# Kernel tuning notes

Measured on AMD Instinct MI355X. Metric: run time of the kernel, lower is better.

## Reference

```python
import jax, jax.numpy as jnp
import numpy as np

DIM_IN, DIM_H, DIM_OUT = 1024, 512, 256
E, T, B = 8, 4, 16384


def setup_inputs() -> dict:
    key = jax.random.key(0)
    ks = jax.random.split(key, 8)
    s1 = 1.0 / np.sqrt(DIM_IN)
    s2 = 1.0 / np.sqrt(DIM_H)
    x = jax.random.normal(ks[0], (B, DIM_IN), dtype=jnp.float32)
    # stacked expert params: layer1 [E, H, IN], layer2 [E, OUT, H]
    W1 = jax.random.uniform(ks[1], (E, DIM_H, DIM_IN), jnp.float32, -s1, s1)
    b1 = jax.random.uniform(ks[2], (E, DIM_H), jnp.float32, -s1, s1)
    W2 = jax.random.uniform(ks[3], (E, DIM_OUT, DIM_H), jnp.float32, -s2, s2)
    b2 = jax.random.uniform(ks[4], (E, DIM_OUT), jnp.float32, -s2, s2)
    # gate params: [T, E, IN]
    Wg = jax.random.uniform(ks[5], (T, E, DIM_IN), jnp.float32, -s1, s1)
    bg = jax.random.uniform(ks[6], (T, E), jnp.float32, -s1, s1)
    return {"x": x, "W1": W1, "b1": b1, "W2": W2, "b2": b2, "Wg": Wg, "bg": bg}


def reference(x, W1, b1, W2, b2, Wg, bg):
    # Experts: Linear+ReLU, Linear+ReLU (dropout=0 / eval mode)
    h = jax.nn.relu(jnp.einsum('bi,ehi->beh', x, W1) + b1)          # [B,E,H]
    feats = jax.nn.relu(jnp.einsum('beh,edh->bed', h, W2) + b2)     # [B,E,D]
    # Gates: softmax over experts, one gate per task
    logits = jnp.einsum('bi,tei->bte', x, Wg) + bg                  # [B,T,E]
    w = jax.nn.softmax(logits, axis=-1)                             # [B,T,E]
    # Weighted combine: einsum('bde,be->bd') per task
    out = jnp.einsum('bed,bte->tbd', feats, w)                      # [T,B,D]
    return out
```

## Files before the change

### kernel.cpp

```cpp
#include <hip/hip_runtime.h>


typedef __attribute__((ext_vector_type(8))) __bf16 bf16x8;
typedef __attribute__((ext_vector_type(4))) float f32x4;
typedef __attribute__((ext_vector_type(8))) unsigned short u16x8;

__device__ __forceinline__ float bf2f(unsigned short u) {
  union { unsigned int i; float f; } x;
  x.i = ((unsigned int)u) << 16;
  return x.f;
}

__device__ __forceinline__ unsigned short f2bf(float f) {
  union { float f; unsigned int i; } x;
  x.f = f;
  unsigned int r = x.i + 0x7FFFu + ((x.i >> 16) & 1u);
  return (unsigned short)(r >> 16);
}

__device__ __forceinline__ void gload_lds16(const unsigned short* g, unsigned short* l) {
  __builtin_amdgcn_global_load_lds(
      (const __attribute__((address_space(1))) void*)g,
      (__attribute__((address_space(3))) void*)l, 16, 0, 0);
}

__global__ void cvt_k(const float* __restrict__ in, unsigned short* __restrict__ out, int n4) {
  int i = blockIdx.x * blockDim.x + threadIdx.x;
  if (i >= n4) return;
  float4 v = ((const float4*)in)[i];
  ushort4 o;
  o.x = f2bf(v.x); o.y = f2bf(v.y); o.z = f2bf(v.z); o.w = f2bf(v.w);
  ((ushort4*)out)[i] = o;
}

__global__ __launch_bounds__(256) void gates_k(
    const unsigned short* __restrict__ xb,
    const unsigned short* __restrict__ Wgb,
    const float* __restrict__ bg,
    float* __restrict__ gw)
{
  const int lane = threadIdx.x & 63;
  const int wid = threadIdx.x >> 6;
  const int wgid = blockIdx.x * 4 + wid;
  const int brow = wgid * 16;
  const int l15 = lane & 15, lhi = lane >> 4;

  f32x4 acc0 = {0.f, 0.f, 0.f, 0.f};
  f32x4 acc1 = {0.f, 0.f, 0.f, 0.f};
  for (int k0 = 0; k0 < 1024; k0 += 32) {
    bf16x8 a  = *(const bf16x8*)&xb[(size_t)(brow + l15) * 1024 + k0 + lhi * 8];
    bf16x8 b0 = *(const bf16x8*)&Wgb[(size_t)l15 * 1024 + k0 + lhi * 8];
    bf16x8 b1 = *(const bf16x8*)&Wgb[(size_t)(16 + l15) * 1024 + k0 + lhi * 8];
    acc0 = __builtin_amdgcn_mfma_f32_16x16x32_bf16(a, b0, acc0, 0, 0, 0);
    acc1 = __builtin_amdgcn_mfma_f32_16x16x32_bf16(a, b1, acc1, 0, 0, 0);
  }
  const float bg0 = bg[l15];
  const float bg1 = bg[16 + l15];
#pragma unroll
  for (int r = 0; r < 4; ++r) {
    float v0 = acc0[r] + bg0;
    float v1 = acc1[r] + bg1;
    float m0 = v0, m1 = v1;
#pragma unroll
    for (int d = 1; d <= 4; d <<= 1) {
      m0 = fmaxf(m0, __shfl_xor(m0, d));
      m1 = fmaxf(m1, __shfl_xor(m1, d));
    }
    float e0 = __expf(v0 - m0), e1 = __expf(v1 - m1);
    float s0 = e0, s1 = e1;
#pragma unroll
    for (int d = 1; d <= 4; d <<= 1) {
      s0 += __shfl_xor(s0, d);
      s1 += __shfl_xor(s1, d);
    }
    int b = brow + lhi * 4 + r;
    gw[(size_t)b * 32 + l15]      = e0 / s0;
    gw[(size_t)b * 32 + 16 + l15] = e1 / s1;
  }
}

template <bool RELU>
__global__ __launch_bounds__(512, 2) void gemm256(
    const unsigned short* __restrict__ A, int lda, int aZ,
    const unsigned short* __restrict__ B,
    const float* __restrict__ bias,
    unsigned short* __restrict__ C, int ldc, int cZ,
    int tilesN, int N, int K)
{
  extern __shared__ char smem_raw[];
  unsigned short* lds = (unsigned short*)smem_raw;
  char* ldsb = (char*)smem_raw;

  const int tid = threadIdx.x;
  const int lane = tid & 63, wid = tid >> 6;
  const int wr = wid >> 2, wc = wid & 3;
  const int l15 = lane & 15, lhi = lane >> 4;

  const int nwg = gridDim.x;
  const int cpx = nwg >> 3;
  const int wg = blockIdx.x;
  const int swz = (wg & 7) * cpx + (wg >> 3);
  const int rt = swz / tilesN, ct = swz - rt * tilesN;
  const int brow = rt * 256, bcol = ct * 256;
  const int e = blockIdx.z;

  const unsigned short* Ab = A + (size_t)e * aZ + (size_t)brow * lda;
  const unsigned short* Bb = B + (size_t)e * N * K + (size_t)bcol * K;
  const float* biasb = bias + (size_t)e * N;
  unsigned short* Cb = C + (size_t)e * cZ;

  const int NT = K >> 6;
  const int NI = NT >> 1;

  const int trow = tid >> 3;
  const int cg8 = (((tid & 7) ^ (trow & 7)) << 3);

  const int axor = (l15 & 7) << 4;
  const int koff0 = (lhi << 4) ^ axor;
  const int koff1 = (64 + (lhi << 4)) ^ axor;

  const char* pA0 = ldsb + wr * 16384 + l15 * 128 + koff0;
  const char* pA1 = ldsb + wr * 16384 + l15 * 128 + koff1;
  const char* pB0 = ldsb + 65536 + wc * 8192 + l15 * 128 + koff0;
  const char* pB1 = ldsb + 65536 + wc * 8192 + l15 * 128 + koff1;

  f32x4 bias4[4];
#pragma unroll
  for (int nf = 0; nf < 4; ++nf)
    bias4[nf] = *(const f32x4*)&biasb[bcol + wc * 64 + nf * 16 + lhi * 4];

  const f32x4 zero = {0.f, 0.f, 0.f, 0.f};
  f32x4 acc[8][4];
#pragma unroll
  for (int m = 0; m < 8; ++m)
#pragma unroll
    for (int n = 0; n < 4; ++n) acc[m][n] = zero;

  auto STAGE_A = [&](int slot, int t, int u) {
    gload_lds16(Ab + (size_t)(u * 64 + trow) * lda + (t * 64 + cg8),
                lds + slot * 16384 + u * 4096 + wid * 512);
  };
  auto STAGE_B = [&](int slot, int t, int u) {
    gload_lds16(Bb + (size_t)(u * 64 + trow) * K + (t * 64 + cg8),
                lds + 32768 + slot * 16384 + u * 4096 + wid * 512);
  };

#pragma unroll
  for (int u = 0; u < 4; ++u) STAGE_B(0, 0, u);
#pragma unroll
  for (int u = 0; u < 4; ++u) STAGE_A(0, 0, u);
  asm volatile("s_waitcnt vmcnt(0)" ::: "memory");
  __builtin_amdgcn_s_barrier();

  auto ktile = [&](int slot, int tn, bool stageNext) {
    bf16x8 af[4][2], bfr[4][2];
#pragma unroll
    for (int mi = 0; mi < 4; ++mi) {
      af[mi][0] = *(const bf16x8*)(pA0 + slot * 32768 + mi * 2048);
      af[mi][1] = *(const bf16x8*)(pA1 + slot * 32768 + mi * 2048);
    }
#pragma unroll
    for (int n = 0; n < 2; ++n) {
      bfr[n][0] = *(const bf16x8*)(pB0 + slot * 32768 + n * 2048);
      bfr[n][1] = *(const bf16x8*)(pB1 + slot * 32768 + n * 2048);
    }
    if (stageNext) { STAGE_B(slot ^ 1, tn, 0); STAGE_B(slot ^ 1, tn, 1); }
    __builtin_amdgcn_s_barrier();
    __builtin_amdgcn_s_setprio(1);
#pragma unroll
    for (int kk = 0; kk < 2; ++kk)
#pragma unroll
      for (int mi = 0; mi < 4; ++mi)
#pragma unroll
        for (int n = 0; n < 2; ++n)
          acc[mi][n] = __builtin_amdgcn_mfma_f32_16x16x32_bf16(bfr[n][kk], af[mi][kk], acc[mi][n], 0, 0, 0);
    __builtin_amdgcn_s_setprio(0);
    __builtin_amdgcn_s_barrier();

#pragma unroll
    for (int n = 0; n < 2; ++n) {
      bfr[2 + n][0] = *(const bf16x8*)(pB0 + slot * 32768 + (2 + n) * 2048);
      bfr[2 + n][1] = *(const bf16x8*)(pB1 + slot * 32768 + (2 + n) * 2048);
    }
    if (stageNext) { STAGE_B(slot ^ 1, tn, 2); STAGE_B(slot ^ 1, tn, 3); }
    __builtin_amdgcn_s_barrier();
    __builtin_amdgcn_s_setprio(1);
#pragma unroll
    for (int kk = 0; kk < 2; ++kk)
#pragma unroll
      for (int mi = 0; mi < 4; ++mi)
#pragma unroll
        for (int n = 0; n < 2; ++n)
          acc[mi][2 + n] = __builtin_amdgcn_mfma_f32_16x16x32_bf16(bfr[2 + n][kk], af[mi][kk], acc[mi][2 + n], 0, 0, 0);
    __builtin_amdgcn_s_setprio(0);
    asm volatile("s_waitcnt vmcnt(4)" ::: "memory");
    __builtin_amdgcn_s_barrier();

#pragma unroll
    for (int mi = 0; mi < 4; ++mi) {
      af[mi][0] = *(const bf16x8*)(pA0 + slot * 32768 + 8192 + mi * 2048);
      af[mi][1] = *(const bf16x8*)(pA1 + slot * 32768 + 8192 + mi * 2048);
    }
    if (stageNext) { STAGE_A(slot ^ 1, tn, 0); STAGE_A(slot ^ 1, tn, 2); }
    __builtin_amdgcn_s_barrier();
    __builtin_amdgcn_s_setprio(1);
#pragma unroll
    for (int kk = 0; kk < 2; ++kk)
#pragma unroll
      for (int mi = 0; mi < 4; ++mi)
#pragma unroll
        for (int n = 0; n < 2; ++n)
          acc[4 + mi][n] = __builtin_amdgcn_mfma_f32_16x16x32_bf16(bfr[n][kk], af[mi][kk], acc[4 + mi][n], 0, 0, 0);
    __builtin_amdgcn_s_setprio(0);
    __builtin_amdgcn_s_barrier();

    if (stageNext) { STAGE_A(slot ^ 1, tn, 1); STAGE_A(slot ^ 1, tn, 3); }
    __builtin_amdgcn_s_barrier();
    __builtin_amdgcn_s_setprio(1);
#pragma unroll
    for (int kk = 0; kk < 2; ++kk)
#pragma unroll
      for (int mi = 0; mi < 4; ++mi)
#pragma unroll
        for (int n = 0; n < 2; ++n)
          acc[4 + mi][2 + n] = __builtin_amdgcn_mfma_f32_16x16x32_bf16(bfr[2 + n][kk], af[mi][kk], acc[4 + mi][2 + n], 0, 0, 0);
    __builtin_amdgcn_s_setprio(0);
    asm volatile("s_waitcnt vmcnt(2)" ::: "memory");
    __builtin_amdgcn_s_barrier();
  };

  for (int i = 0; i < NI; ++i) {
    ktile(0, 2 * i + 1, true);
    ktile(1, 2 * i + 2, (2 * i + 2) < NT);
  }

#pragma unroll
  for (int mf = 0; mf < 8; ++mf) {
    const size_t rowoff = (size_t)(brow + wr * 128 + mf * 16 + l15) * ldc;
#pragma unroll
    for (int nf = 0; nf < 4; ++nf) {
      const int col = bcol + wc * 64 + nf * 16 + lhi * 4;
      f32x4 v = acc[mf][nf];
      ushort4 o;
      float v0 = v[0] + bias4[nf][0];
      float v1 = v[1] + bias4[nf][1];
      float v2 = v[2] + bias4[nf][2];
      float v3 = v[3] + bias4[nf][3];
      if (RELU) {
        v0 = v0 > 0.f ? v0 : 0.f;
        v1 = v1 > 0.f ? v1 : 0.f;
        v2 = v2 > 0.f ? v2 : 0.f;
        v3 = v3 > 0.f ? v3 : 0.f;
      }
      o.x = f2bf(v0); o.y = f2bf(v1); o.z = f2bf(v2); o.w = f2bf(v3);
      *(ushort4*)&Cb[rowoff + col] = o;
    }
  }
}

__global__ __launch_bounds__(256) void combine_k(
    const unsigned short* __restrict__ feats,
    const float* __restrict__ gw,
    float* __restrict__ out)
{
  int tid = blockIdx.x * 256 + threadIdx.x;
  int b = tid >> 5;
  int d0 = (tid & 31) * 8;

  const f32x4* wv4 = (const f32x4*)(gw + (size_t)b * 32);
  f32x4 wv[8];
#pragma unroll
  for (int i = 0; i < 8; ++i) wv[i] = wv4[i];

  float o[4][8];
#pragma unroll
  for (int t = 0; t < 4; ++t)
#pragma unroll
    for (int j = 0; j < 8; ++j) o[t][j] = 0.f;

#pragma unroll
  for (int e = 0; e < 8; ++e) {
    u16x8 fv = *(const u16x8*)&feats[((size_t)b * 8 + e) * 256 + d0];
    float f[8];
#pragma unroll
    for (int j = 0; j < 8; ++j) f[j] = bf2f(fv[j]);
#pragma unroll
    for (int t = 0; t < 4; ++t) {
      float wt = wv[(t * 8 + e) >> 2][(t * 8 + e) & 3];
#pragma unroll
      for (int j = 0; j < 8; ++j) o[t][j] += wt * f[j];
    }
  }
#pragma unroll
  for (int t = 0; t < 4; ++t) {
    f32x4* dst = (f32x4*)(out + ((size_t)t * 16384 + b) * 256 + d0);
    f32x4 s0 = {o[t][0], o[t][1], o[t][2], o[t][3]};
    f32x4 s1 = {o[t][4], o[t][5], o[t][6], o[t][7]};
    dst[0] = s0;
    dst[1] = s1;
  }
}

extern "C" void kernel_launch(void* const* d_in, const int* in_sizes, int n_in,
                              void* d_out, int out_size, void* d_ws, size_t ws_size,
                              hipStream_t stream) {
  (void)in_sizes; (void)n_in; (void)out_size; (void)ws_size;
  const float* x  = (const float*)d_in[0];
  const float* W1 = (const float*)d_in[1];
  const float* b1 = (const float*)d_in[2];
  const float* W2 = (const float*)d_in[3];
  const float* b2 = (const float*)d_in[4];
  const float* Wg = (const float*)d_in[5];
  const float* bg = (const float*)d_in[6];
  float* out = (float*)d_out;

  char* ws = (char*)d_ws;
  unsigned short* xb    = (unsigned short*)ws; ws += (size_t)16384 * 1024 * 2;
  unsigned short* W1b   = (unsigned short*)ws; ws += (size_t)4096 * 1024 * 2;
  unsigned short* W2b   = (unsigned short*)ws; ws += (size_t)2048 * 512 * 2;
  unsigned short* Wgb   = (unsigned short*)ws; ws += (size_t)32 * 1024 * 2;
  float*          gw    = (float*)ws;         ws += (size_t)16384 * 32 * 4;
  unsigned short* H     = (unsigned short*)ws; ws += (size_t)16384 * 4096 * 2;
  unsigned short* feats = (unsigned short*)ws; ws += (size_t)16384 * 2048 * 2;

  cvt_k<<<16384, 256, 0, stream>>>(x, xb, 16384 * 1024 / 4);
  cvt_k<<<4096, 256, 0, stream>>>(W1, W1b, 4096 * 1024 / 4);
  cvt_k<<<1024, 256, 0, stream>>>(W2, W2b, 2048 * 512 / 4);
  cvt_k<<<32, 256, 0, stream>>>(Wg, Wgb, 32 * 1024 / 4);

  gates_k<<<256, 256, 0, stream>>>(xb, Wgb, bg, gw);

  gemm256<true><<<dim3(1024, 1, 1), 512, 131072, stream>>>(
      xb, 1024, 0, W1b, b1, H, 4096, 0, 16, 4096, 1024);

  gemm256<true><<<dim3(64, 1, 8), 512, 131072, stream>>>(
      H, 4096, 512, W2b, b2, feats, 2048, 256, 1, 256, 512);

  combine_k<<<2048, 256, 0, stream>>>(feats, gw, out);
}
```

Measured before the change: 278.6 us.

## Restage gemm256 pipeline to prefetch B two tiles ahead; use simpler GEMM for layer 2

Reorders the gemm256 main loop so the next A tile is staged into the other slot while the B tile two steps ahead is staged into the current slot. Prologue loads and waitcnt thresholds change to match, and the bias load moves after the loop. The second-layer GEMM switches to a new 128x128 single-buffered kernel with 256 threads, which gives it more blocks for the small N=256 problem. The risks are wrong waitcnt accounting in the new schedule and slower non-coalesced scalar stores in the new kernel.

Result: slower. 285.6 us (+2.5%).

```diff
diff --git a/kernel.cpp b/kernel.cpp
--- a/kernel.cpp
+++ b/kernel.cpp
@@ -124,11 +124,6 @@
   const char* pB0 = ldsb + 65536 + wc * 8192 + l15 * 128 + koff0;
   const char* pB1 = ldsb + 65536 + wc * 8192 + l15 * 128 + koff1;
 
-  f32x4 bias4[4];
-#pragma unroll
-  for (int nf = 0; nf < 4; ++nf)
-    bias4[nf] = *(const f32x4*)&biasb[bcol + wc * 64 + nf * 16 + lhi * 4];
-
   const f32x4 zero = {0.f, 0.f, 0.f, 0.f};
   f32x4 acc[8][4];
 #pragma unroll
@@ -147,13 +142,18 @@
 
 #pragma unroll
   for (int u = 0; u < 4; ++u) STAGE_B(0, 0, u);
-#pragma unroll
-  for (int u = 0; u < 4; ++u) STAGE_A(0, 0, u);
-  asm volatile("s_waitcnt vmcnt(0)" ::: "memory");
+  STAGE_A(0, 0, 0); STAGE_A(0, 0, 2);
+  STAGE_A(0, 0, 1); STAGE_A(0, 0, 3);
+#pragma unroll
+  for (int u = 0; u < 4; ++u) STAGE_B(1, 1, u);
+  asm volatile("s_waitcnt vmcnt(6)" ::: "memory");
   __builtin_amdgcn_s_barrier();
 
-  auto ktile = [&](int slot, int tn, bool stageNext) {
+  auto ktile = [&](int slot, int t) {
+    const bool stA = (t + 1) < NT;
+    const bool stB = (t + 2) < NT;
     bf16x8 af[4][2], bfr[4][2];
+
 #pragma unroll
     for (int mi = 0; mi < 4; ++mi) {
       af[mi][0] = *(const bf16x8*)(pA0 + slot * 32768 + mi * 2048);
@@ -164,7 +164,7 @@
       bfr[n][0] = *(const bf16x8*)(pB0 + slot * 32768 + n * 2048);
       bfr[n][1] = *(const bf16x8*)(pB1 + slot * 32768 + n * 2048);
     }
-    if (stageNext) { STAGE_B(slot ^ 1, tn, 0); STAGE_B(slot ^ 1, tn, 1); }
+    if (stA) { STAGE_A(slot ^ 1, t + 1, 0); STAGE_A(slot ^ 1, t + 1, 2); }
     __builtin_amdgcn_s_barrier();
     __builtin_amdgcn_s_setprio(1);
 #pragma unroll
@@ -182,7 +182,7 @@
       bfr[2 + n][0] = *(const bf16x8*)(pB0 + slot * 32768 + (2 + n) * 2048);
       bfr[2 + n][1] = *(const bf16x8*)(pB1 + slot * 32768 + (2 + n) * 2048);
     }
-    if (stageNext) { STAGE_B(slot ^ 1, tn, 2); STAGE_B(slot ^ 1, tn, 3); }
+    if (stA) { STAGE_A(slot ^ 1, t + 1, 1); STAGE_A(slot ^ 1, t + 1, 3); }
     __builtin_amdgcn_s_barrier();
     __builtin_amdgcn_s_setprio(1);
 #pragma unroll
@@ -193,7 +193,8 @@
         for (int n = 0; n < 2; ++n)
           acc[mi][2 + n] = __builtin_amdgcn_mfma_f32_16x16x32_bf16(bfr[2 + n][kk], af[mi][kk], acc[mi][2 + n], 0, 0, 0);
     __builtin_amdgcn_s_setprio(0);
-    asm volatile("s_waitcnt vmcnt(4)" ::: "memory");
+    if (stA) asm volatile("s_waitcnt vmcnt(8)" ::: "memory");
+    else     asm volatile("s_waitcnt vmcnt(0)" ::: "memory");
     __builtin_amdgcn_s_barrier();
 
 #pragma unroll
@@ -201,7 +202,7 @@
       af[mi][0] = *(const bf16x8*)(pA0 + slot * 32768 + 8192 + mi * 2048);
       af[mi][1] = *(const bf16x8*)(pA1 + slot * 32768 + 8192 + mi * 2048);
     }
-    if (stageNext) { STAGE_A(slot ^ 1, tn, 0); STAGE_A(slot ^ 1, tn, 2); }
+    if (stB) { STAGE_B(slot, t + 2, 0); STAGE_B(slot, t + 2, 1); }
     __builtin_amdgcn_s_barrier();
     __builtin_amdgcn_s_setprio(1);
 #pragma unroll
@@ -214,7 +215,7 @@
     __builtin_amdgcn_s_setprio(0);
     __builtin_amdgcn_s_barrier();
 
-    if (stageNext) { STAGE_A(slot ^ 1, tn, 1); STAGE_A(slot ^ 1, tn, 3); }
+    if (stB) { STAGE_B(slot, t + 2, 2); STAGE_B(slot, t + 2, 3); }
     __builtin_amdgcn_s_barrier();
     __builtin_amdgcn_s_setprio(1);
 #pragma unroll
@@ -225,14 +226,25 @@
         for (int n = 0; n < 2; ++n)
           acc[4 + mi][2 + n] = __builtin_amdgcn_mfma_f32_16x16x32_bf16(bfr[2 + n][kk], af[mi][kk], acc[4 + mi][2 + n], 0, 0, 0);
     __builtin_amdgcn_s_setprio(0);
-    asm volatile("s_waitcnt vmcnt(2)" ::: "memory");
-    __builtin_amdgcn_s_barrier();
+    if (stB) {
+      asm volatile("s_waitcnt vmcnt(6)" ::: "memory");
+      __builtin_amdgcn_s_barrier();
+    } else if (stA) {
+      asm volatile("s_waitcnt vmcnt(2)" ::: "memory");
+      __builtin_amdgcn_s_barrier();
+    }
   };
 
+#pragma unroll 1
   for (int i = 0; i < NI; ++i) {
-    ktile(0, 2 * i + 1, true);
-    ktile(1, 2 * i + 2, (2 * i + 2) < NT);
-  }
+    ktile(0, 2 * i);
+    ktile(1, 2 * i + 1);
+  }
+
+  f32x4 bias4[4];
+#pragma unroll
+  for (int nf = 0; nf < 4; ++nf)
+    bias4[nf] = *(const f32x4*)&biasb[bcol + wc * 64 + nf * 16 + lhi * 4];
 
 #pragma unroll
   for (int mf = 0; mf < 8; ++mf) {
@@ -258,6 +270,88 @@
   }
 }
 
+template <bool RELU>
+__global__ __launch_bounds__(256) void gemm_bt(
+    const unsigned short* __restrict__ A, int lda, int aZ,
+    const unsigned short* __restrict__ B,
+    const float* __restrict__ bias,
+    unsigned short* __restrict__ C, int ldc, int cZ,
+    int N, int K)
+{
+  __shared__ unsigned short As[128 * 64];
+  __shared__ unsigned short Bs[128 * 64];
+  const int tid = threadIdx.x;
+  const int wid = tid >> 6;
+  const int lane = tid & 63;
+  const int wr = wid >> 1, wc = wid & 1;
+  const int l15 = lane & 15, lhi = lane >> 4;
+  const int brow = blockIdx.x * 128;
+  const int bcol = blockIdx.y * 128;
+  const int e = blockIdx.z;
+
+  const unsigned short* Ab = A + (size_t)e * aZ;
+  const unsigned short* Bb = B + (size_t)e * N * K;
+  const float* biasb = bias + (size_t)e * N;
+  unsigned short* Cb = C + (size_t)e * cZ;
+
+  const f32x4 zero = {0.f, 0.f, 0.f, 0.f};
+  f32x4 acc[4][4];
+#pragma unroll
+  for (int m = 0; m < 4; ++m)
+#pragma unroll
+    for (int n = 0; n < 4; ++n) acc[m][n] = zero;
+
+  const int srow = lane >> 3;
+  const int scol = (lane & 7) * 8;
+  const int rbase = wid * 32;
+
+  for (int k0 = 0; k0 < K; k0 += 64) {
+#pragma unroll
+    for (int i = 0; i < 4; ++i) {
+      int r = rbase + i * 8;
+      gload_lds16(Ab + (size_t)(brow + r + srow) * lda + (k0 + scol), &As[r * 64]);
+    }
+#pragma unroll
+    for (int i = 0; i < 4; ++i) {
+      int r = rbase + i * 8;
+      gload_lds16(Bb + (size_t)(bcol + r + srow) * K + (k0 + scol), &Bs[r * 64]);
+    }
+    __syncthreads();
+#pragma unroll
+    for (int kk = 0; kk < 2; ++kk) {
+      bf16x8 af[4], bfr[4];
+#pragma unroll
+      for (int m = 0; m < 4; ++m)
+        af[m] = *(const bf16x8*)&As[(wr * 64 + m * 16 + l15) * 64 + kk * 32 + lhi * 8];
+#pragma unroll
+      for (int n = 0; n < 4; ++n)
+        bfr[n] = *(const bf16x8*)&Bs[(wc * 64 + n * 16 + l15) * 64 + kk * 32 + lhi * 8];
+#pragma unroll
+      for (int m = 0; m < 4; ++m)
+#pragma unroll
+        for (int n = 0; n < 4; ++n)
+          acc[m][n] = __builtin_amdgcn_mfma_f32_16x16x32_bf16(af[m], bfr[n], acc[m][n], 0, 0, 0);
+    }
+    __syncthreads();
+  }
+
+#pragma unroll
+  for (int n = 0; n < 4; ++n) {
+    int col = bcol + wc * 64 + n * 16 + l15;
+    float bv = biasb[col];
+#pragma unroll
+    for (int m = 0; m < 4; ++m) {
+      int row0 = brow + wr * 64 + m * 16 + lhi * 4;
+#pragma unroll
+      for (int r = 0; r < 4; ++r) {
+        float v = acc[m][n][r] + bv;
+        if (RELU) v = v > 0.f ? v : 0.f;
+        Cb[(size_t)(row0 + r) * ldc + col] = f2bf(v);
+      }
+    }
+  }
+}
+
 __global__ __launch_bounds__(256) void combine_k(
     const unsigned short* __restrict__ feats,
     const float* __restrict__ gw,
@@ -333,8 +427,8 @@
   gemm256<true><<<dim3(1024, 1, 1), 512, 131072, stream>>>(
       xb, 1024, 0, W1b, b1, H, 4096, 0, 16, 4096, 1024);
 
-  gemm256<true><<<dim3(64, 1, 8), 512, 131072, stream>>>(
-      H, 4096, 512, W2b, b2, feats, 2048, 256, 1, 256, 512);
+  gemm_bt<true><<<dim3(128, 2, 8), 256, 0, stream>>>(
+      H, 4096, 512, W2b, b2, feats, 2048, 256, 256, 512);
 
   combine_k<<<2048, 256, 0, stream>>>(feats, gw, out);
 }
```

## Fuse second expert GEMM with gated combine, dropping feats buffer

Applied to the files above, without the earlier changes.

Replaces the batched layer-2 GEMM and the separate combine kernel with one kernel. Each block computes 64 rows by 128 output columns for all 8 experts, applies bias and ReLU, and accumulates the gate-weighted sum into per-task registers. This removes the write and re-read of the bf16 feats intermediate and one launch. In exchange it uses a much smaller tile with one barrier per 64-wide K chunk and reads W2 directly from global memory, which may lower MFMA efficiency. It also adds `unroll 1` on the main GEMM loop.

Result: slower. 367.8 us (+32.0%).

```diff
diff --git a/kernel.cpp b/kernel.cpp
--- a/kernel.cpp
+++ b/kernel.cpp
@@ -3,7 +3,6 @@
 
 typedef __attribute__((ext_vector_type(8))) __bf16 bf16x8;
 typedef __attribute__((ext_vector_type(4))) float f32x4;
-typedef __attribute__((ext_vector_type(8))) unsigned short u16x8;
 
 __device__ __forceinline__ float bf2f(unsigned short u) {
   union { unsigned int i; float f; } x;
@@ -229,6 +228,7 @@
     __builtin_amdgcn_s_barrier();
   };
 
+#pragma unroll 1
   for (int i = 0; i < NI; ++i) {
     ktile(0, 2 * i + 1, true);
     ktile(1, 2 * i + 2, (2 * i + 2) < NT);
@@ -258,47 +258,128 @@
   }
 }
 
-__global__ __launch_bounds__(256) void combine_k(
-    const unsigned short* __restrict__ feats,
+__global__ __launch_bounds__(512) void expert2_combine_k(
+    const unsigned short* __restrict__ H,
+    const unsigned short* __restrict__ W2b,
+    const float* __restrict__ b2,
     const float* __restrict__ gw,
     float* __restrict__ out)
 {
-  int tid = blockIdx.x * 256 + threadIdx.x;
-  int b = tid >> 5;
-  int d0 = (tid & 31) * 8;
-
-  const f32x4* wv4 = (const f32x4*)(gw + (size_t)b * 32);
-  f32x4 wv[8];
-#pragma unroll
-  for (int i = 0; i < 8; ++i) wv[i] = wv4[i];
-
-  float o[4][8];
+  __shared__ unsigned short Hs[2][64 * 64];
+  __shared__ float gws[32 * 64];
+
+  const int tid = threadIdx.x;
+  const int lane = tid & 63, wid = tid >> 6;
+  const int wr = wid >> 2, wc = wid & 3;
+  const int l15 = lane & 15, lhi = lane >> 4;
+  const int brow = blockIdx.x * 64;
+  const int bcol = blockIdx.y * 128;
+
+  for (int i = tid; i < 64 * 32; i += 512) {
+    int r = i & 63, c = i >> 6;
+    gws[c * 64 + r] = gw[(size_t)(brow + r) * 32 + c];
+  }
+
+  const int trow = tid >> 3;
+  const int cg8 = (((tid & 7) ^ (trow & 7)) << 3);
+  const unsigned short* Hb = H + (size_t)brow * 4096;
+
+  const int axor = (l15 & 7) << 4;
+  const char* pH = (const char*)Hs + (wr * 32 + l15) * 128;
+  const int koff0 = (0 + (lhi << 4)) ^ axor;
+  const int koff1 = (64 + (lhi << 4)) ^ axor;
+
+  const f32x4 zero = {0.f, 0.f, 0.f, 0.f};
+  f32x4 oacc[4][2][2];
 #pragma unroll
   for (int t = 0; t < 4; ++t)
 #pragma unroll
-    for (int j = 0; j < 8; ++j) o[t][j] = 0.f;
-
-#pragma unroll
+    for (int m = 0; m < 2; ++m)
+#pragma unroll
+      for (int n = 0; n < 2; ++n) oacc[t][m][n] = zero;
+
+  auto STAGE = [&](int buf, int e, int c) {
+    gload_lds16(Hb + (size_t)trow * 4096 + (e * 512 + c * 64 + cg8),
+                &Hs[buf][wid * 512]);
+  };
+
+  STAGE(0, 0, 0);
+  __syncthreads();
+
+#pragma unroll 1
   for (int e = 0; e < 8; ++e) {
-    u16x8 fv = *(const u16x8*)&feats[((size_t)b * 8 + e) * 256 + d0];
-    float f[8];
-#pragma unroll
-    for (int j = 0; j < 8; ++j) f[j] = bf2f(fv[j]);
+    f32x4 g[2][2];
+#pragma unroll
+    for (int m = 0; m < 2; ++m)
+#pragma unroll
+      for (int n = 0; n < 2; ++n) g[m][n] = zero;
+
+#pragma unroll
+    for (int c = 0; c < 8; ++c) {
+      const int cc = e * 8 + c;
+      const int buf = c & 1;
+      if (cc + 1 < 64) STAGE((c + 1) & 1, (cc + 1) >> 3, (cc + 1) & 7);
+
+      bf16x8 bfr[2][2];
+#pragma unroll
+      for (int n = 0; n < 2; ++n) {
+        const size_t wrow = (size_t)(e * 256 + bcol + wc * 32 + n * 16 + l15) * 512;
+        bfr[n][0] = *(const bf16x8*)&W2b[wrow + c * 64 + lhi * 8];
+        bfr[n][1] = *(const bf16x8*)&W2b[wrow + c * 64 + 32 + lhi * 8];
+      }
+      bf16x8 af[2][2];
+#pragma unroll
+      for (int m = 0; m < 2; ++m) {
+        af[m][0] = *(const bf16x8*)(pH + buf * 8192 + m * 2048 + koff0);
+        af[m][1] = *(const bf16x8*)(pH + buf * 8192 + m * 2048 + koff1);
+      }
+#pragma unroll
+      for (int kk = 0; kk < 2; ++kk)
+#pragma unroll
+        for (int m = 0; m < 2; ++m)
+#pragma unroll
+          for (int n = 0; n < 2; ++n)
+            g[m][n] = __builtin_amdgcn_mfma_f32_16x16x32_bf16(bfr[n][kk], af[m][kk], g[m][n], 0, 0, 0);
+      __syncthreads();
+    }
+
+#pragma unroll
+    for (int n = 0; n < 2; ++n) {
+      f32x4 bv = *(const f32x4*)&b2[e * 256 + bcol + wc * 32 + n * 16 + lhi * 4];
+#pragma unroll
+      for (int m = 0; m < 2; ++m) {
+        f32x4 v = g[m][n];
+#pragma unroll
+        for (int r = 0; r < 4; ++r) {
+          float f = v[r] + bv[r];
+          v[r] = f > 0.f ? f : 0.f;
+        }
+        g[m][n] = v;
+      }
+    }
 #pragma unroll
     for (int t = 0; t < 4; ++t) {
-      float wt = wv[(t * 8 + e) >> 2][(t * 8 + e) & 3];
-#pragma unroll
-      for (int j = 0; j < 8; ++j) o[t][j] += wt * f[j];
-    }
-  }
-#pragma unroll
-  for (int t = 0; t < 4; ++t) {
-    f32x4* dst = (f32x4*)(out + ((size_t)t * 16384 + b) * 256 + d0);
-    f32x4 s0 = {o[t][0], o[t][1], o[t][2], o[t][3]};
-    f32x4 s1 = {o[t][4], o[t][5], o[t][6], o[t][7]};
-    dst[0] = s0;
-    dst[1] = s1;
-  }
+#pragma unroll
+      for (int m = 0; m < 2; ++m) {
+        float gwt = gws[(t * 8 + e) * 64 + wr * 32 + m * 16 + l15];
+#pragma unroll
+        for (int n = 0; n < 2; ++n)
+#pragma unroll
+          for (int r = 0; r < 4; ++r)
+            oacc[t][m][n][r] += gwt * g[m][n][r];
+      }
+    }
+  }
+
+#pragma unroll
+  for (int t = 0; t < 4; ++t)
+#pragma unroll
+    for (int m = 0; m < 2; ++m) {
+      const size_t rowoff = ((size_t)t * 16384 + brow + wr * 32 + m * 16 + l15) * 256;
+#pragma unroll
+      for (int n = 0; n < 2; ++n)
+        *(f32x4*)&out[rowoff + bcol + wc * 32 + n * 16 + lhi * 4] = oacc[t][m][n];
+    }
 }
 
 extern "C" void kernel_launch(void* const* d_in, const int* in_sizes, int n_in,
@@ -321,7 +402,6 @@
   unsigned short* Wgb   = (unsigned short*)ws; ws += (size_t)32 * 1024 * 2;
   float*          gw    = (float*)ws;         ws += (size_t)16384 * 32 * 4;
   unsigned short* H     = (unsigned short*)ws; ws += (size_t)16384 * 4096 * 2;
-  unsigned short* feats = (unsigned short*)ws; ws += (size_t)16384 * 2048 * 2;
 
   cvt_k<<<16384, 256, 0, stream>>>(x, xb, 16384 * 1024 / 4);
   cvt_k<<<4096, 256, 0, stream>>>(W1, W1b, 4096 * 1024 / 4);
@@ -333,8 +413,5 @@
   gemm256<true><<<dim3(1024, 1, 1), 512, 131072, stream>>>(
       xb, 1024, 0, W1b, b1, H, 4096, 0, 16, 4096, 1024);
 
-  gemm256<true><<<dim3(64, 1, 8), 512, 131072, stream>>>(
-      H, 4096, 512, W2b, b2, feats, 2048, 256, 1, 256, 512);
-
-  combine_k<<<2048, 256, 0, stream>>>(feats, gw, out);
-}
+  expert2_combine_k<<<dim3(256, 2, 1), 512, 0, stream>>>(H, W2b, b2, gw, out);
+}
```
